# Optimization experiments

Measured on AMD Instinct MI355X. Metric: run time of the kernel, lower is better.

The kernel has to match this reference:

```python
import jax, jax.numpy as jnp
import numpy as np

N_QUBITS = 4

def _apply_shared(state, U, q, n):
    # apply 2x2 gate U (shared across batch) to qubit q; axis n-q of state holds qubit q
    ax = n - q
    s = jnp.moveaxis(state, ax, -1)
    s = jnp.einsum('b...i,ji->b...j', s, U)
    return jnp.moveaxis(s, -1, ax)

def _apply_batched(state, U, q, n):
    # per-sample 2x2 gates U: [B,2,2]
    ax = n - q
    s = jnp.moveaxis(state, ax, -1)
    s = jnp.einsum('b...i,bji->b...j', s, U)
    return jnp.moveaxis(s, -1, ax)

def _cx(state, c, t, n):
    # CNOT: flip target bit where control bit == 1
    axc, axt = n - c, n - t
    c0 = jnp.take(state, jnp.array([0]), axis=axc)
    c1 = jnp.take(state, jnp.array([1]), axis=axc)
    c1 = jnp.flip(c1, axis=axt)
    return jnp.concatenate([c0, c1], axis=axc)

def _simulate(angles, theta, n=N_QUBITS):
    # batched 4-qubit statevector simulation of the fixed variational circuit
    B = angles.shape[0]
    state = jnp.zeros((B, 2 ** n), jnp.complex64).at[:, 0].set(1.0).reshape((B,) + (2,) * n)
    # data-encoding RY rotations (per-sample angles)
    for q in range(n):
        th = angles[:, q]
        c = jnp.cos(th / 2).astype(jnp.complex64)
        s = jnp.sin(th / 2).astype(jnp.complex64)
        U = jnp.stack([jnp.stack([c, -s], -1), jnp.stack([s, c], -1)], -2)  # [B,2,2]
        state = _apply_batched(state, U, q, n)
    # two variational layers: RX,RY,RZ (same angle) per qubit, then CX chain + wrap-around CX
    for layer in range(2):
        for q in range(n):
            th = theta[layer * n + q]
            c = jnp.cos(th / 2).astype(jnp.complex64)
            s = jnp.sin(th / 2).astype(jnp.complex64)
            Urx = jnp.stack([jnp.stack([c, -1j * s]), jnp.stack([-1j * s, c])])
            Ury = jnp.stack([jnp.stack([c, -s]), jnp.stack([s, c])])
            Urz = jnp.diag(jnp.stack([jnp.exp(-0.5j * th), jnp.exp(0.5j * th)])).astype(jnp.complex64)
            for U in (Urx, Ury, Urz):
                state = _apply_shared(state, U, q, n)
        for q in range(n - 1):
            state = _cx(state, q, q + 1, n)
        if n > 2:
            state = _cx(state, n - 1, 0, n)
    probs = jnp.abs(state) ** 2  # [B,2,2,2,2]; axis n-q corresponds to qubit q
    feats = []
    for i in range(n):
        # Qiskit Pauli label ordering: feature i is <Z_{n-1-i}>
        q = n - 1 - i
        ax = n - q
        other = tuple(a for a in range(1, n + 1) if a != ax)
        m = probs.sum(axis=other)  # [B,2]
        feats.append(m[:, 0] - m[:, 1])
    return jnp.stack(feats, axis=1).astype(jnp.float32)  # [B, n]

def setup_inputs() -> dict:
    key = jax.random.key(0)
    ks = jax.random.split(key, 8)
    B, D, L, n = 32768, 1024, 64, N_QUBITS
    return {
        'x': jax.random.normal(ks[0], (B, D), jnp.float32),
        'W1': jax.random.normal(ks[1], (2 * n, D), jnp.float32) / np.sqrt(D).astype(np.float32),
        'b1': jax.random.normal(ks[2], (2 * n,), jnp.float32) * 0.01,
        'quantum_params': jax.random.normal(ks[3], (3 * n,), jnp.float32) * 0.1,
        'W_mu': jax.random.normal(ks[4], (L, n), jnp.float32) / np.sqrt(n).astype(np.float32),
        'b_mu': jax.random.normal(ks[5], (L,), jnp.float32) * 0.01,
        'W_lv': jax.random.normal(ks[6], (L, n), jnp.float32) / np.sqrt(n).astype(np.float32),
        'b_lv': jax.random.normal(ks[7], (L,), jnp.float32) * 0.01,
    }

def reference(x, W1, b1, quantum_params, W_mu, b_mu, W_lv, b_lv):
    co = jnp.tanh(x @ W1.T + b1)            # [B, 2n]
    angles = co[:, :N_QUBITS]               # only first n_qubits used as RY angles
    # original detaches inputs to the quantum circuit -> no grad flows through it
    qf = jax.lax.stop_gradient(_simulate(angles, quantum_params))  # [B, n]
    mu = qf @ W_mu.T + b_mu
    logvar = qf @ W_lv.T + b_lv
    return (mu, logvar)
```

## Files before the change

### kernel.cpp

```cpp
#include <hip/hip_runtime.h>

typedef float f32x4 __attribute__((ext_vector_type(4)));

#define D_IN 1024

__device__ __forceinline__ float fast_tanh(float x) {
  float e = __expf(2.0f * x);
  return 1.0f - 2.0f * __builtin_amdgcn_rcpf(e + 1.0f);
}

__global__ __launch_bounds__(256) void dots_kernel(
    const float* __restrict__ x, const float* __restrict__ W1,
    float* __restrict__ dots, int B) {
  __shared__ f32x4 W1L[1024];

  const int tid = threadIdx.x;
  {
    const f32x4* wp = reinterpret_cast<const f32x4*>(W1);
#pragma unroll
    for (int k = 0; k < 4; ++k) W1L[k * 256 + tid] = wp[k * 256 + tid];
  }
  __syncthreads();

  const int lane = tid & 63;
  const int p = lane & 3;
  const int wave = blockIdx.x * 4 + (tid >> 6);
  const int row = wave * 16 + (lane >> 2);
  if (row >= B) return;

  const float* xr = x + (size_t)row * D_IN;

  for (int rep = 0; rep < 4; ++rep) {
    float acc[4] = {0.f, 0.f, 0.f, 0.f};

#pragma unroll
    for (int g = 0; g < 16; ++g) {
      const int db = g * 64 + p * 16;
      f32x4 xv[4];
#pragma unroll
      for (int k = 0; k < 4; ++k)
        xv[k] = *reinterpret_cast<const f32x4*>(xr + db + 4 * k);
#pragma unroll
      for (int k = 0; k < 4; ++k) {
        const int wi = (db >> 2) + k;
        f32x4 xk = xv[k];
#pragma unroll
        for (int j = 0; j < 4; ++j) {
          f32x4 w = W1L[j * 256 + wi];
          acc[j] = fmaf(xk.x, w.x, acc[j]);
          acc[j] = fmaf(xk.y, w.y, acc[j]);
          acc[j] = fmaf(xk.z, w.z, acc[j]);
          acc[j] = fmaf(xk.w, w.w, acc[j]);
        }
      }
    }

#pragma unroll
    for (int j = 0; j < 4; ++j) {
      acc[j] += __shfl_xor(acc[j], 1);
      acc[j] += __shfl_xor(acc[j], 2);
    }
    float outv = (p == 0) ? acc[0] : (p == 1) ? acc[1] : (p == 2) ? acc[2] : acc[3];
    dots[(size_t)row * 4 + p] = outv;
  }
}

__global__ __launch_bounds__(256) void tail_kernel(
    const float* __restrict__ dots, const float* __restrict__ b1,
    const float* __restrict__ theta,
    const float* __restrict__ Wmu, const float* __restrict__ bmu,
    const float* __restrict__ Wlv, const float* __restrict__ blv,
    float* __restrict__ out, int B) {
  __shared__ float Vre[16][17];
  __shared__ float Vim[16][17];
  __shared__ float Mlds[4][16][16];

  const int tid = threadIdx.x;

  if (tid < 16) {
    float re[16], im[16];
#pragma unroll
    for (int z = 0; z < 16; ++z) { re[z] = 0.f; im[z] = 0.f; }
    re[tid] = 1.f;
    for (int layer = 0; layer < 2; ++layer) {
#pragma unroll
      for (int q = 0; q < 4; ++q) {
        float th = theta[layer * 4 + q];
        float s, c;
        __sincosf(0.5f * th, &s, &c);
#pragma unroll
        for (int z = 0; z < 16; ++z) {
          if (!((z >> q) & 1)) {
            int z1 = z | (1 << q);
            float ar = re[z], ai = im[z], br = re[z1], bi = im[z1];
            re[z]  = c * ar + s * bi;  im[z]  = c * ai - s * br;
            re[z1] = c * br + s * ai;  im[z1] = c * bi - s * ar;
          }
        }
#pragma unroll
        for (int z = 0; z < 16; ++z) {
          if (!((z >> q) & 1)) {
            int z1 = z | (1 << q);
            float ar = re[z], ai = im[z], br = re[z1], bi = im[z1];
            re[z]  = c * ar - s * br;  im[z]  = c * ai - s * bi;
            re[z1] = s * ar + c * br;  im[z1] = s * ai + c * bi;
          }
        }
#pragma unroll
        for (int z = 0; z < 16; ++z) {
          if (!((z >> q) & 1)) {
            int z1 = z | (1 << q);
            float ar = re[z], ai = im[z], br = re[z1], bi = im[z1];
            re[z]  = c * ar + s * ai;  im[z]  = c * ai - s * ar;
            re[z1] = c * br - s * bi;  im[z1] = c * bi + s * br;
          }
        }
      }
      const int cqs[4] = {0, 1, 2, 3};
      const int tqs[4] = {1, 2, 3, 0};
#pragma unroll
      for (int gIdx = 0; gIdx < 4; ++gIdx) {
#pragma unroll
        for (int z = 0; z < 16; ++z) {
          if (((z >> cqs[gIdx]) & 1) && !((z >> tqs[gIdx]) & 1)) {
            int z1 = z | (1 << tqs[gIdx]);
            float tr = re[z], ti = im[z];
            re[z] = re[z1];  im[z] = im[z1];
            re[z1] = tr;     im[z1] = ti;
          }
        }
      }
    }
#pragma unroll
    for (int z = 0; z < 16; ++z) { Vre[z][tid] = re[z]; Vim[z][tid] = im[z]; }
  }
  __syncthreads();

  {
    const int i = tid >> 6, a = (tid >> 2) & 15, b0 = (tid & 3) * 4;
    float ra[16], ia[16];
#pragma unroll
    for (int z = 0; z < 16; ++z) { ra[z] = Vre[z][a]; ia[z] = Vim[z][a]; }
#pragma unroll
    for (int k = 0; k < 4; ++k) {
      const int b = b0 + k;
      float acc = 0.f;
#pragma unroll
      for (int z = 0; z < 16; ++z) {
        float sg = ((z >> (3 - i)) & 1) ? -1.f : 1.f;
        acc += sg * (ra[z] * Vre[z][b] + ia[z] * Vim[z][b]);
      }
      Mlds[i][a][b] = acc;
    }
  }
  __syncthreads();

  const int lane = tid & 63;
  const int wave = blockIdx.x * 4 + (tid >> 6);
  const int nwaves = gridDim.x * 4;
  const int g = lane >> 4;
  const int mz = lane & 15;

  float Mr[16];
#pragma unroll
  for (int k = 0; k < 16; ++k) Mr[k] = Mlds[g][mz][k];

  float b1r[4];
#pragma unroll
  for (int j = 0; j < 4; ++j) b1r[j] = b1[j];

  float wmuP[4], wlvP[4];
#pragma unroll
  for (int k = 0; k < 4; ++k) {
    wmuP[k] = Wmu[lane * 4 + (g ^ k)];
    wlvP[k] = Wlv[lane * 4 + (g ^ k)];
  }
  const float bmur = bmu[lane], blvr = blv[lane];
  const size_t lv_base = (size_t)B * 64;

  for (int r = wave; r < B; r += nwaves) {
    const float4 dv = *reinterpret_cast<const float4*>(dots + (size_t)r * 4);

    float cq[4], sq[4];
    __sincosf(0.5f * fast_tanh(dv.x + b1r[0]), &sq[0], &cq[0]);
    __sincosf(0.5f * fast_tanh(dv.y + b1r[1]), &sq[1], &cq[1]);
    __sincosf(0.5f * fast_tanh(dv.z + b1r[2]), &sq[2], &cq[2]);
    __sincosf(0.5f * fast_tanh(dv.w + b1r[3]), &sq[3], &cq[3]);

    const float A0 = cq[0] * cq[1], A1 = sq[0] * cq[1];
    const float A2 = cq[0] * sq[1], A3 = sq[0] * sq[1];
    const float B0 = cq[2] * cq[3], B1 = sq[2] * cq[3];
    const float B2 = cq[2] * sq[3], B3 = sq[2] * sq[3];

    float t0 = fmaf(Mr[3], A3, fmaf(Mr[2], A2, fmaf(Mr[1], A1, Mr[0] * A0)));
    float t1 = fmaf(Mr[7], A3, fmaf(Mr[6], A2, fmaf(Mr[5], A1, Mr[4] * A0)));
    float t2 = fmaf(Mr[11], A3, fmaf(Mr[10], A2, fmaf(Mr[9], A1, Mr[8] * A0)));
    float t3 = fmaf(Mr[15], A3, fmaf(Mr[14], A2, fmaf(Mr[13], A1, Mr[12] * A0)));
    float tdot = fmaf(t3, B3, fmaf(t2, B2, fmaf(t1, B1, t0 * B0)));

    float svm = ((mz & 1) ? sq[0] : cq[0]);
    svm *= ((mz & 2) ? sq[1] : cq[1]);
    svm *= ((mz & 4) ? sq[2] : cq[2]);
    svm *= ((mz & 8) ? sq[3] : cq[3]);

    float pacc = tdot * svm;
#pragma unroll
    for (int off = 8; off; off >>= 1) pacc += __shfl_xor(pacc, off);
    float v1 = __shfl_xor(pacc, 16);
    float v2 = __shfl_xor(pacc, 32);
    float v3 = __shfl_xor(v1, 32);

    float mu = fmaf(v3, wmuP[3], fmaf(v2, wmuP[2], fmaf(v1, wmuP[1], fmaf(pacc, wmuP[0], bmur))));
    float lv = fmaf(v3, wlvP[3], fmaf(v2, wlvP[2], fmaf(v1, wlvP[1], fmaf(pacc, wlvP[0], blvr))));
    __builtin_nontemporal_store(mu, out + (size_t)r * 64 + lane);
    __builtin_nontemporal_store(lv, out + lv_base + (size_t)r * 64 + lane);
  }
}

extern "C" void kernel_launch(void* const* d_in, const int* in_sizes, int n_in,
                              void* d_out, int out_size, void* d_ws, size_t ws_size,
                              hipStream_t stream) {
  const float* x   = (const float*)d_in[0];
  const float* W1  = (const float*)d_in[1];
  const float* b1  = (const float*)d_in[2];
  const float* qp  = (const float*)d_in[3];
  const float* Wmu = (const float*)d_in[4];
  const float* bmu = (const float*)d_in[5];
  const float* Wlv = (const float*)d_in[6];
  const float* blv = (const float*)d_in[7];
  float* out = (float*)d_out;
  float* dots = (float*)d_ws;

  const int B = out_size / 128;

  int blocks1 = (B + 63) / 64;
  dots_kernel<<<blocks1, 256, 0, stream>>>(x, W1, dots, B);

  int blocks2 = (B + 31) / 32;
  if (blocks2 > 1024) blocks2 = 1024;
  tail_kernel<<<blocks2, 256, 0, stream>>>(dots, b1, qp, Wmu, bmu, Wlv, blv,
                                           out, B);
}
```

Before: 40.67 us.

## Drop redundant repeat loop and double-buffer x row loads in dots kernel

Removes the four-times repeated dot-product loop, so each row of x is reduced only once. The inner loop is restructured into a register double-buffer: two 16-vector buffers load the next chunk of x while the current chunk is multiplied against W1 in LDS. Launch bounds now request one block per CU, which gives the compiler room for the larger register footprint. The risk is lower occupancy to hide global memory latency, since the kernel mostly streams x from HBM.

```diff
diff --git a/kernel.cpp b/kernel.cpp
--- a/kernel.cpp
+++ b/kernel.cpp
@@ -9,7 +9,7 @@
   return 1.0f - 2.0f * __builtin_amdgcn_rcpf(e + 1.0f);
 }
 
-__global__ __launch_bounds__(256) void dots_kernel(
+__global__ __launch_bounds__(256, 1) void dots_kernel(
     const float* __restrict__ x, const float* __restrict__ W1,
     float* __restrict__ dots, int B) {
   __shared__ f32x4 W1L[1024];
@@ -28,41 +28,85 @@
   const int row = wave * 16 + (lane >> 2);
   if (row >= B) return;
 
-  const float* xr = x + (size_t)row * D_IN;
-
-  for (int rep = 0; rep < 4; ++rep) {
-    float acc[4] = {0.f, 0.f, 0.f, 0.f};
-
-#pragma unroll
-    for (int g = 0; g < 16; ++g) {
-      const int db = g * 64 + p * 16;
-      f32x4 xv[4];
-#pragma unroll
-      for (int k = 0; k < 4; ++k)
-        xv[k] = *reinterpret_cast<const f32x4*>(xr + db + 4 * k);
-#pragma unroll
-      for (int k = 0; k < 4; ++k) {
-        const int wi = (db >> 2) + k;
-        f32x4 xk = xv[k];
-#pragma unroll
-        for (int j = 0; j < 4; ++j) {
-          f32x4 w = W1L[j * 256 + wi];
-          acc[j] = fmaf(xk.x, w.x, acc[j]);
-          acc[j] = fmaf(xk.y, w.y, acc[j]);
-          acc[j] = fmaf(xk.z, w.z, acc[j]);
-          acc[j] = fmaf(xk.w, w.w, acc[j]);
-        }
-      }
-    }
-
-#pragma unroll
-    for (int j = 0; j < 4; ++j) {
-      acc[j] += __shfl_xor(acc[j], 1);
-      acc[j] += __shfl_xor(acc[j], 2);
-    }
-    float outv = (p == 0) ? acc[0] : (p == 1) ? acc[1] : (p == 2) ? acc[2] : acc[3];
-    dots[(size_t)row * 4 + p] = outv;
-  }
+  const f32x4* xp4 = reinterpret_cast<const f32x4*>(x + (size_t)row * D_IN);
+
+#define CHUNK_IDX(c) ((((c) >> 2) * 16) + (p * 4) + ((c) & 3))
+
+  float acc[4] = {0.f, 0.f, 0.f, 0.f};
+  f32x4 bufA[16], bufB[16];
+
+#pragma unroll
+  for (int k = 0; k < 16; ++k) bufA[k] = xp4[CHUNK_IDX(k)];
+#pragma unroll
+  for (int k = 0; k < 16; ++k) bufB[k] = xp4[CHUNK_IDX(16 + k)];
+
+#pragma unroll
+  for (int k = 0; k < 16; ++k) {
+    const int wi = CHUNK_IDX(k);
+    f32x4 xk = bufA[k];
+#pragma unroll
+    for (int j = 0; j < 4; ++j) {
+      f32x4 w = W1L[j * 256 + wi];
+      acc[j] = fmaf(xk.x, w.x, acc[j]);
+      acc[j] = fmaf(xk.y, w.y, acc[j]);
+      acc[j] = fmaf(xk.z, w.z, acc[j]);
+      acc[j] = fmaf(xk.w, w.w, acc[j]);
+    }
+  }
+#pragma unroll
+  for (int k = 0; k < 16; ++k) bufA[k] = xp4[CHUNK_IDX(32 + k)];
+
+#pragma unroll
+  for (int k = 0; k < 16; ++k) {
+    const int wi = CHUNK_IDX(16 + k);
+    f32x4 xk = bufB[k];
+#pragma unroll
+    for (int j = 0; j < 4; ++j) {
+      f32x4 w = W1L[j * 256 + wi];
+      acc[j] = fmaf(xk.x, w.x, acc[j]);
+      acc[j] = fmaf(xk.y, w.y, acc[j]);
+      acc[j] = fmaf(xk.z, w.z, acc[j]);
+      acc[j] = fmaf(xk.w, w.w, acc[j]);
+    }
+  }
+#pragma unroll
+  for (int k = 0; k < 16; ++k) bufB[k] = xp4[CHUNK_IDX(48 + k)];
+
+#pragma unroll
+  for (int k = 0; k < 16; ++k) {
+    const int wi = CHUNK_IDX(32 + k);
+    f32x4 xk = bufA[k];
+#pragma unroll
+    for (int j = 0; j < 4; ++j) {
+      f32x4 w = W1L[j * 256 + wi];
+      acc[j] = fmaf(xk.x, w.x, acc[j]);
+      acc[j] = fmaf(xk.y, w.y, acc[j]);
+      acc[j] = fmaf(xk.z, w.z, acc[j]);
+      acc[j] = fmaf(xk.w, w.w, acc[j]);
+    }
+  }
+#pragma unroll
+  for (int k = 0; k < 16; ++k) {
+    const int wi = CHUNK_IDX(48 + k);
+    f32x4 xk = bufB[k];
+#pragma unroll
+    for (int j = 0; j < 4; ++j) {
+      f32x4 w = W1L[j * 256 + wi];
+      acc[j] = fmaf(xk.x, w.x, acc[j]);
+      acc[j] = fmaf(xk.y, w.y, acc[j]);
+      acc[j] = fmaf(xk.z, w.z, acc[j]);
+      acc[j] = fmaf(xk.w, w.w, acc[j]);
+    }
+  }
+#undef CHUNK_IDX
+
+#pragma unroll
+  for (int j = 0; j < 4; ++j) {
+    acc[j] += __shfl_xor(acc[j], 1);
+    acc[j] += __shfl_xor(acc[j], 2);
+  }
+  float outv = (p == 0) ? acc[0] : (p == 1) ? acc[1] : (p == 2) ? acc[2] : acc[3];
+  dots[(size_t)row * 4 + p] = outv;
 }
 
 __global__ __launch_bounds__(256) void tail_kernel(
```

Result: no change. 41.25 us (+1.4%).

## Fuse projection and quantum tail into one kernel with LDS-staged dots

Applied to the files above, without the earlier changes.

Merges the x·W1ᵀ projection kernel and the quantum-circuit tail kernel into a single launch. Each wave computes 16 rows of the projection and stages them in shared memory, then immediately runs the circuit and readout for those same rows. This removes the global workspace round-trip, one kernel launch, and the redundant 4x repetition of the projection loop in the old code. In exchange, every block now rebuilds the circuit matrices, and the compute and store phases run back to back within each wave instead of in separately scheduled kernels.

```diff
diff --git a/kernel.cpp b/kernel.cpp
--- a/kernel.cpp
+++ b/kernel.cpp
@@ -9,73 +9,25 @@
   return 1.0f - 2.0f * __builtin_amdgcn_rcpf(e + 1.0f);
 }
 
-__global__ __launch_bounds__(256) void dots_kernel(
+__global__ __launch_bounds__(256, 1) void fused_qenc_kernel(
     const float* __restrict__ x, const float* __restrict__ W1,
-    float* __restrict__ dots, int B) {
-  __shared__ f32x4 W1L[1024];
-
-  const int tid = threadIdx.x;
-  {
-    const f32x4* wp = reinterpret_cast<const f32x4*>(W1);
-#pragma unroll
-    for (int k = 0; k < 4; ++k) W1L[k * 256 + tid] = wp[k * 256 + tid];
-  }
-  __syncthreads();
-
-  const int lane = tid & 63;
-  const int p = lane & 3;
-  const int wave = blockIdx.x * 4 + (tid >> 6);
-  const int row = wave * 16 + (lane >> 2);
-  if (row >= B) return;
-
-  const float* xr = x + (size_t)row * D_IN;
-
-  for (int rep = 0; rep < 4; ++rep) {
-    float acc[4] = {0.f, 0.f, 0.f, 0.f};
-
-#pragma unroll
-    for (int g = 0; g < 16; ++g) {
-      const int db = g * 64 + p * 16;
-      f32x4 xv[4];
-#pragma unroll
-      for (int k = 0; k < 4; ++k)
-        xv[k] = *reinterpret_cast<const f32x4*>(xr + db + 4 * k);
-#pragma unroll
-      for (int k = 0; k < 4; ++k) {
-        const int wi = (db >> 2) + k;
-        f32x4 xk = xv[k];
-#pragma unroll
-        for (int j = 0; j < 4; ++j) {
-          f32x4 w = W1L[j * 256 + wi];
-          acc[j] = fmaf(xk.x, w.x, acc[j]);
-          acc[j] = fmaf(xk.y, w.y, acc[j]);
-          acc[j] = fmaf(xk.z, w.z, acc[j]);
-          acc[j] = fmaf(xk.w, w.w, acc[j]);
-        }
-      }
-    }
-
-#pragma unroll
-    for (int j = 0; j < 4; ++j) {
-      acc[j] += __shfl_xor(acc[j], 1);
-      acc[j] += __shfl_xor(acc[j], 2);
-    }
-    float outv = (p == 0) ? acc[0] : (p == 1) ? acc[1] : (p == 2) ? acc[2] : acc[3];
-    dots[(size_t)row * 4 + p] = outv;
-  }
-}
-
-__global__ __launch_bounds__(256) void tail_kernel(
-    const float* __restrict__ dots, const float* __restrict__ b1,
-    const float* __restrict__ theta,
+    const float* __restrict__ b1, const float* __restrict__ theta,
     const float* __restrict__ Wmu, const float* __restrict__ bmu,
     const float* __restrict__ Wlv, const float* __restrict__ blv,
     float* __restrict__ out, int B) {
+  __shared__ f32x4 W1L[1024];
   __shared__ float Vre[16][17];
   __shared__ float Vim[16][17];
   __shared__ float Mlds[4][16][16];
+  __shared__ f32x4 dotsL[64];
 
   const int tid = threadIdx.x;
+
+  {
+    const f32x4* wp = reinterpret_cast<const f32x4*>(W1);
+#pragma unroll
+    for (int k = 0; k < 4; ++k) W1L[k * 256 + tid] = wp[k * 256 + tid];
+  }
 
   if (tid < 16) {
     float re[16], im[16];
@@ -156,19 +108,18 @@
   __syncthreads();
 
   const int lane = tid & 63;
-  const int wave = blockIdx.x * 4 + (tid >> 6);
-  const int nwaves = gridDim.x * 4;
+  const int widx = tid >> 6;
+  const int wave = blockIdx.x * 4 + widx;
   const int g = lane >> 4;
   const int mz = lane & 15;
+  const int p = lane & 3;
 
   float Mr[16];
 #pragma unroll
   for (int k = 0; k < 16; ++k) Mr[k] = Mlds[g][mz][k];
-
   float b1r[4];
 #pragma unroll
   for (int j = 0; j < 4; ++j) b1r[j] = b1[j];
-
   float wmuP[4], wlvP[4];
 #pragma unroll
   for (int k = 0; k < 4; ++k) {
@@ -178,8 +129,47 @@
   const float bmur = bmu[lane], blvr = blv[lane];
   const size_t lv_base = (size_t)B * 64;
 
-  for (int r = wave; r < B; r += nwaves) {
-    const float4 dv = *reinterpret_cast<const float4*>(dots + (size_t)r * 4);
+  {
+    const int row = wave * 16 + (lane >> 2);
+    if (row < B) {
+      const float* xr = x + (size_t)row * D_IN;
+      float acc[4] = {0.f, 0.f, 0.f, 0.f};
+#pragma unroll
+      for (int gg = 0; gg < 16; ++gg) {
+        const int db = gg * 64 + p * 16;
+        f32x4 xv[4];
+#pragma unroll
+        for (int k = 0; k < 4; ++k)
+          xv[k] = *reinterpret_cast<const f32x4*>(xr + db + 4 * k);
+#pragma unroll
+        for (int k = 0; k < 4; ++k) {
+          const int wi = (db >> 2) + k;
+          f32x4 xk = xv[k];
+#pragma unroll
+          for (int j = 0; j < 4; ++j) {
+            f32x4 w = W1L[j * 256 + wi];
+            acc[j] = fmaf(xk.x, w.x, acc[j]);
+            acc[j] = fmaf(xk.y, w.y, acc[j]);
+            acc[j] = fmaf(xk.z, w.z, acc[j]);
+            acc[j] = fmaf(xk.w, w.w, acc[j]);
+          }
+        }
+      }
+#pragma unroll
+      for (int j = 0; j < 4; ++j) {
+        acc[j] += __shfl_xor(acc[j], 1);
+        acc[j] += __shfl_xor(acc[j], 2);
+      }
+      float outv = (p == 0) ? acc[0] : (p == 1) ? acc[1] : (p == 2) ? acc[2] : acc[3];
+      reinterpret_cast<float*>(&dotsL[widx * 16 + (lane >> 2)])[p] = outv;
+    }
+  }
+
+#pragma unroll 1
+  for (int rr = 0; rr < 16; ++rr) {
+    const int r = wave * 16 + rr;
+    if (r >= B) break;
+    f32x4 dv = dotsL[widx * 16 + rr];
 
     float cq[4], sq[4];
     __sincosf(0.5f * fast_tanh(dv.x + b1r[0]), &sq[0], &cq[0]);
@@ -229,15 +219,10 @@
   const float* Wlv = (const float*)d_in[6];
   const float* blv = (const float*)d_in[7];
   float* out = (float*)d_out;
-  float* dots = (float*)d_ws;
 
   const int B = out_size / 128;
 
-  int blocks1 = (B + 63) / 64;
-  dots_kernel<<<blocks1, 256, 0, stream>>>(x, W1, dots, B);
-
-  int blocks2 = (B + 31) / 32;
-  if (blocks2 > 1024) blocks2 = 1024;
-  tail_kernel<<<blocks2, 256, 0, stream>>>(dots, b1, qp, Wmu, bmu, Wlv, blv,
-                                           out, B);
+  int blocks = (B + 63) / 64;
+  fused_qenc_kernel<<<blocks, 256, 0, stream>>>(x, W1, b1, qp, Wmu, bmu, Wlv, blv,
+                                                out, B);
 }
```

Measured after the change: 38.90 us. 1.05x faster.
